# Optimization experiments

Hardware: AMD Instinct MI355X
Metric: run time of the kernel (lower is better)

## Reference

```python
import jax, jax.numpy as jnp
import numpy as np


def _up2(x):
    return jnp.repeat(jnp.repeat(x, 2, axis=2), 2, axis=3)


def setup_inputs() -> dict:
    key = jax.random.key(0)
    ks = jax.random.split(key, 6)
    Vps, C, H, W = 32, 128, 64, 64
    return {
        "x1": jax.random.normal(ks[0], (Vps, C, H, W), dtype=jnp.float32),
        "x2": jax.random.normal(ks[1], (Vps, C, H // 2, W // 2), dtype=jnp.float32),
        "x3": jax.random.normal(ks[2], (Vps, C, H // 4, W // 4), dtype=jnp.float32),
        "x4": jax.random.normal(ks[3], (Vps, C, H // 4, W // 4), dtype=jnp.float32),
        "conv_w": jax.random.normal(ks[4], (128, 512), dtype=jnp.float32) * 0.02,
        "conv_b": jnp.zeros((128,), dtype=jnp.float32),
        "gamma": jnp.zeros((1,), dtype=jnp.float32),
        "weight": jnp.ones((128,), dtype=jnp.float32),
        "lin_w": jax.random.normal(ks[5], (1, 128), dtype=jnp.float32) * 0.1,
    }


def reference(x1, x2, x3, x4, conv_w, conv_b, gamma, weight, lin_w):
    # upsample lower pyramid levels to x1 resolution and concat on channels
    x_sm = jnp.concatenate([x1, _up2(x2), _up2(_up2(x3)), _up2(_up2(x4))], axis=1)
    # 1x1 conv: [Vps,512,H,W] x [128,512] -> [Vps,128,H,W]
    x_sm = jnp.einsum('vchw,oc->vohw', x_sm, conv_w) + conv_b[None, :, None, None]
    Vps, C, H, W = x_sm.shape

    # --- batch (viewport) attention ---
    gap = jnp.mean(x_sm, axis=(2, 3))                     # [Vps, C]
    v_q = gap @ lin_w.T                                    # [Vps, 1]
    att = v_q @ v_q.T                                      # [Vps, Vps]
    att_new = jnp.broadcast_to(jnp.max(att, axis=-1, keepdims=True), att.shape)
    vps_mat = jax.nn.softmax(att_new, axis=-1)             # rows constant -> uniform
    v_v = x_sm.reshape(Vps, C * H * W)
    vps_att = (vps_mat @ v_v).reshape(Vps, C, H, W)
    x_sm = vps_att * gamma + x_sm

    # --- channel attention ---
    c_q = jnp.mean(x_sm, axis=(2, 3))                      # [Vps, C]
    att_C = c_q.T @ c_q                                    # [C, C]
    C_mat = jax.nn.softmax(att_C, axis=-1) * weight        # broadcast over last dim
    c_v = x_sm.reshape(C, Vps * H * W)                     # faithful raw reshape as in torch
    C_att = (C_mat @ c_v).reshape(Vps, C, H, W)
    out = C_att + x_sm
    return out.reshape(Vps, C, H * W)
```

## Files before the change

kernel.cpp:

```cpp
#include <hip/hip_runtime.h>

#define V 32
#define CH 128
#define SP 4096

typedef __attribute__((ext_vector_type(8))) short bf16x8;
typedef __attribute__((ext_vector_type(4))) float f32x4;

__device__ __forceinline__ unsigned short bf16rne(float x) {
    union { float f; unsigned u; } v; v.f = x;
    unsigned r = v.u + 0x7fff + ((v.u >> 16) & 1);
    return (unsigned short)(r >> 16);
}

__device__ __forceinline__ int xswz(int s) { return (s & 7) ^ ((s >> 2) & 7); }

__device__ __forceinline__ const float* xsm_row(const float* xsm, int j, int r) {
    return xsm + ((size_t)((j >> 2) * CH + (j & 3) * 32 + r)) * SP;
}

__global__ __launch_bounds__(256) void prep_w(const float* __restrict__ W,
                                              unsigned short* __restrict__ Wpad)
{
    int row = blockIdx.x;
    int j = threadIdx.x;
    if (j < 136) {
        int sigma = row >> 7, o = row & 127;
        float v = (j < 128) ? W[o * 512 + sigma * 128 + j] : 0.f;
        Wpad[row * 136 + j] = bf16rne(v);
    }
}

__global__ __launch_bounds__(256, 3) void conv_lo(
    const float* __restrict__ xa, const float* __restrict__ xb,
    const unsigned short* __restrict__ WA, const unsigned short* __restrict__ WB,
    int spatial, int nph, float* __restrict__ outbuf)
{
    __shared__ __align__(16) unsigned short Xl[64 * 128];
    const int v = blockIdx.y, sc = blockIdx.x, tid = threadIdx.x;
    const int lane = tid & 63, w = tid >> 6;
    const int l15 = lane & 15, quad = lane >> 4;
    const int o0 = (w >> 1) * 64, s0 = (w & 1) * 32;
    const int sq = tid & 15, cp0 = tid >> 4;

    f32x4 acc[4][2];
#pragma unroll
    for (int it = 0; it < 4; ++it)
#pragma unroll
        for (int st = 0; st < 2; ++st) acc[it][st] = (f32x4){0.f, 0.f, 0.f, 0.f};

#pragma unroll 1
    for (int ph = 0; ph < nph; ++ph) {
        if (ph) __syncthreads();
        const float* xp = ph ? xb : xa;
        const unsigned short* wp = ph ? WB : WA;
        bf16x8 af[4][4];
#pragma unroll
        for (int ks = 0; ks < 4; ++ks)
#pragma unroll
            for (int it = 0; it < 4; ++it)
                af[ks][it] = *(const bf16x8*)&wp[(o0 + it * 16 + l15) * 136 + ks * 32 + quad * 8];
        const float* xbase = xp + (size_t)v * CH * spatial + sc * 64;
#pragma unroll
        for (int rep = 0; rep < 4; ++rep) {
            int c = (cp0 + rep * 16) * 2;
            const float* r0 = xbase + (size_t)c * spatial + sq * 4;
            float4 va = *(const float4*)r0;
            float4 vb = *(const float4*)(r0 + spatial);
            float a4[4] = {va.x, va.y, va.z, va.w};
            float b4[4] = {vb.x, vb.y, vb.z, vb.w};
#pragma unroll
            for (int i = 0; i < 4; ++i) {
                int s = sq * 4 + i;
                ushort2 pk; pk.x = bf16rne(a4[i]); pk.y = bf16rne(b4[i]);
                *(ushort2*)&Xl[s * 128 + (((c >> 3) ^ xswz(s)) * 8) + (c & 7)] = pk;
            }
        }
        __syncthreads();
#pragma unroll
        for (int ks = 0; ks < 4; ++ks) {
            int kb = ks * 4 + quad;
            bf16x8 bfr[2];
#pragma unroll
            for (int st = 0; st < 2; ++st) {
                int s = s0 + st * 16 + l15;
                bfr[st] = *(const bf16x8*)&Xl[s * 128 + ((kb ^ xswz(s)) * 8)];
            }
#pragma unroll
            for (int it = 0; it < 4; ++it)
#pragma unroll
                for (int st = 0; st < 2; ++st)
                    acc[it][st] = __builtin_amdgcn_mfma_f32_16x16x32_bf16(
                        bfr[st], af[ks][it], acc[it][st], 0, 0, 0);
        }
    }
#pragma unroll
    for (int it = 0; it < 4; ++it) {
        int o = o0 + it * 16 + l15;
        float* orow = outbuf + ((size_t)(v * CH + o)) * spatial + sc * 64;
#pragma unroll
        for (int st = 0; st < 2; ++st) {
            int sb = s0 + st * 16 + quad * 4;
            *(f32x4*)(orow + sb) = acc[it][st];
        }
    }
}

__global__ __launch_bounds__(256, 2) void conv_full(
    const float* __restrict__ x1, const unsigned short* __restrict__ W0,
    const float* __restrict__ bias, const float* __restrict__ conv2,
    const float* __restrict__ conv34, float* __restrict__ xsm,
    float* __restrict__ gap)
{
    __shared__ __align__(16) unsigned short Xl[2][64 * 128];
    const int vg = blockIdx.y, sc = blockIdx.x, tid = threadIdx.x;
    const int lane = tid & 63, w = tid >> 6;
    const int l15 = lane & 15, quad = lane >> 4;
    const int o0 = (w >> 1) * 64, s0 = (w & 1) * 32;
    const int sq = tid & 15, cp0 = tid >> 4;

    bf16x8 af[4][4];
#pragma unroll
    for (int ks = 0; ks < 4; ++ks)
#pragma unroll
        for (int it = 0; it < 4; ++it)
            af[ks][it] = *(const bf16x8*)&W0[(o0 + it * 16 + l15) * 136 + ks * 32 + quad * 8];
    float bv[4];
#pragma unroll
    for (int it = 0; it < 4; ++it) bv[it] = bias[o0 + it * 16 + l15];

    float4 xva[4], xvb[4];
    {
        const float* xbase = x1 + (size_t)(vg * 4) * CH * SP + sc * 64;
#pragma unroll
        for (int rep = 0; rep < 4; ++rep) {
            int c = (cp0 + rep * 16) * 2;
            const float* r0 = xbase + (size_t)c * SP + sq * 4;
            xva[rep] = *(const float4*)r0;
            xvb[rep] = *(const float4*)(r0 + SP);
        }
    }
#pragma unroll
    for (int rep = 0; rep < 4; ++rep) {
        int c = (cp0 + rep * 16) * 2;
        float a4[4] = {xva[rep].x, xva[rep].y, xva[rep].z, xva[rep].w};
        float b4[4] = {xvb[rep].x, xvb[rep].y, xvb[rep].z, xvb[rep].w};
#pragma unroll
        for (int i = 0; i < 4; ++i) {
            int s = sq * 4 + i;
            ushort2 pk; pk.x = bf16rne(a4[i]); pk.y = bf16rne(b4[i]);
            *(ushort2*)&Xl[0][s * 128 + (((c >> 3) ^ xswz(s)) * 8) + (c & 7)] = pk;
        }
    }

#pragma unroll 1
    for (int t = 0; t < 4; ++t) {
        const int v = vg * 4 + t;
        __syncthreads();
        if (t < 3) {
            const float* xbase = x1 + (size_t)(v + 1) * CH * SP + sc * 64;
#pragma unroll
            for (int rep = 0; rep < 4; ++rep) {
                int c = (cp0 + rep * 16) * 2;
                const float* r0 = xbase + (size_t)c * SP + sq * 4;
                xva[rep] = *(const float4*)r0;
                xvb[rep] = *(const float4*)(r0 + SP);
            }
        }
        const float* c2row = conv2 + (size_t)v * CH * 1024 + (sc >> 1) * 32;
        const float* c34row = conv34 + (size_t)v * CH * 256 + (sc >> 2) * 16;
        float2 c2v[4][2]; float c34v[4][2];
#pragma unroll
        for (int it = 0; it < 4; ++it) {
            int o = o0 + it * 16 + l15;
#pragma unroll
            for (int st = 0; st < 2; ++st) {
                int sb = s0 + st * 16 + quad * 4;
                c2v[it][st] = *(const float2*)(c2row + (size_t)o * 1024 + (sb >> 1));
                c34v[it][st] = c34row[(size_t)o * 256 + (sb >> 2)];
            }
        }
        f32x4 acc[4][2];
#pragma unroll
        for (int it = 0; it < 4; ++it)
#pragma unroll
            for (int st = 0; st < 2; ++st) acc[it][st] = (f32x4){0.f, 0.f, 0.f, 0.f};
        const unsigned short* Xcur = &Xl[t & 1][0];
#pragma unroll
        for (int ks = 0; ks < 4; ++ks) {
            int kb = ks * 4 + quad;
            bf16x8 bfr[2];
#pragma unroll
            for (int st = 0; st < 2; ++st) {
                int s = s0 + st * 16 + l15;
                bfr[st] = *(const bf16x8*)&Xcur[s * 128 + ((kb ^ xswz(s)) * 8)];
            }
#pragma unroll
            for (int it = 0; it < 4; ++it)
#pragma unroll
                for (int st = 0; st < 2; ++st)
                    acc[it][st] = __builtin_amdgcn_mfma_f32_16x16x32_bf16(
                        bfr[st], af[ks][it], acc[it][st], 0, 0, 0);
        }
        float gs[4];
#pragma unroll
        for (int it = 0; it < 4; ++it) {
            int o = o0 + it * 16 + l15;
            float b = bv[it];
            float* orow = xsm + ((size_t)(v * CH + o)) * SP + sc * 64;
            float lsum = 0.f;
#pragma unroll
            for (int st = 0; st < 2; ++st) {
                int sb = s0 + st * 16 + quad * 4;
                f32x4 a = acc[it][st];
                f32x4 ov;
                ov[0] = a[0] + b + c2v[it][st].x + c34v[it][st];
                ov[1] = a[1] + b + c2v[it][st].x + c34v[it][st];
                ov[2] = a[2] + b + c2v[it][st].y + c34v[it][st];
                ov[3] = a[3] + b + c2v[it][st].y + c34v[it][st];
                *(f32x4*)(orow + sb) = ov;
                lsum += ov[0] + ov[1] + ov[2] + ov[3];
            }
            gs[it] = lsum;
        }
#pragma unroll
        for (int m = 16; m < 64; m <<= 1)
#pragma unroll
            for (int k = 0; k < 4; ++k) gs[k] += __shfl_xor(gs[k], m, 64);
        if (quad == 0) {
#pragma unroll
            for (int it = 0; it < 4; ++it)
                atomicAdd(&gap[v * CH + o0 + it * 16 + l15], gs[it]);
        }
        if (t < 3) {
#pragma unroll
            for (int rep = 0; rep < 4; ++rep) {
                int c = (cp0 + rep * 16) * 2;
                float a4[4] = {xva[rep].x, xva[rep].y, xva[rep].z, xva[rep].w};
                float b4[4] = {xvb[rep].x, xvb[rep].y, xvb[rep].z, xvb[rep].w};
#pragma unroll
                for (int i = 0; i < 4; ++i) {
                    int s = sq * 4 + i;
                    ushort2 pk; pk.x = bf16rne(a4[i]); pk.y = bf16rne(b4[i]);
                    *(ushort2*)&Xl[(t + 1) & 1][s * 128 + (((c >> 3) ^ xswz(s)) * 8) + (c & 7)] = pk;
                }
            }
        }
    }
}

__global__ __launch_bounds__(128) void build_G(
    const float* __restrict__ gap, const float* __restrict__ gammap,
    const float* __restrict__ weight, unsigned short* __restrict__ GsPad)
{
    __shared__ float cq[32][128];
    __shared__ float red[128];
    const int i = blockIdx.x, j = threadIdx.x;
    const float g = gammap[0];

    float gb = 0.f;
    for (int v = 0; v < 32; ++v) gb += gap[v * CH + j];
    gb = gb * (1.f / 32.f) * (1.f / 4096.f) * g;
    for (int v = 0; v < 32; ++v) cq[v][j] = gap[v * CH + j] * (1.f / 4096.f) + gb;
    __syncthreads();

    float a = 0.f;
    for (int v = 0; v < 32; ++v) a += cq[v][i] * cq[v][j];

    red[j] = a; __syncthreads();
    float m = -1e30f;
    for (int t = 0; t < 128; ++t) m = fmaxf(m, red[t]);
    __syncthreads();
    float e = __expf(a - m);
    red[j] = e; __syncthreads();
    float ssum = 0.f;
    for (int t = 0; t < 128; ++t) ssum += red[t];
    float cm = e / ssum * weight[j] + ((i == j) ? 1.f : 0.f);
    __syncthreads();
    red[j] = cm; __syncthreads();
    float rs = 0.f;
    for (int t = (j & 3); t < 128; t += 4) rs += red[t];
    float gfull = cm + g * (1.f / 32.f) * rs;
    GsPad[i * 136 + j] = bf16rne(gfull - ((i == j) ? 1.f : 0.f));
}

__global__ __launch_bounds__(256, 2) void apply_G(
    float* __restrict__ xsm, const unsigned short* __restrict__ GsPad)
{
    __shared__ __align__(16) unsigned short Xl[2][64 * 128];
    const int r = blockIdx.y, scg = blockIdx.x, tid = threadIdx.x;
    const int lane = tid & 63, w = tid >> 6;
    const int l15 = lane & 15, quad = lane >> 4;
    const int i0 = (w >> 1) * 64, s0 = (w & 1) * 32;
    const int sq = tid & 15, cp0 = tid >> 4;

    bf16x8 af[4][4];
#pragma unroll
    for (int ks = 0; ks < 4; ++ks)
#pragma unroll
        for (int it = 0; it < 4; ++it)
            af[ks][it] = *(const bf16x8*)&GsPad[(i0 + it * 16 + l15) * 136 + ks * 32 + quad * 8];

    float4 xva[4], xvb[4];
    {
        const int sc = scg * 4;
#pragma unroll
        for (int rep = 0; rep < 4; ++rep) {
            int c = (cp0 + rep * 16) * 2;
            xva[rep] = *(const float4*)(xsm_row(xsm, c, r) + sc * 64 + sq * 4);
            xvb[rep] = *(const float4*)(xsm_row(xsm, c + 1, r) + sc * 64 + sq * 4);
        }
    }
#pragma unroll
    for (int rep = 0; rep < 4; ++rep) {
        int c = (cp0 + rep * 16) * 2;
        float a4[4] = {xva[rep].x, xva[rep].y, xva[rep].z, xva[rep].w};
        float b4[4] = {xvb[rep].x, xvb[rep].y, xvb[rep].z, xvb[rep].w};
#pragma unroll
        for (int i = 0; i < 4; ++i) {
            int s = sq * 4 + i;
            ushort2 pk; pk.x = bf16rne(a4[i]); pk.y = bf16rne(b4[i]);
            *(ushort2*)&Xl[0][s * 128 + (((c >> 3) ^ xswz(s)) * 8) + (c & 7)] = pk;
        }
    }

#pragma unroll 1
    for (int t = 0; t < 4; ++t) {
        const int sc = scg * 4 + t;
        __syncthreads();
        if (t < 3) {
#pragma unroll
            for (int rep = 0; rep < 4; ++rep) {
                int c = (cp0 + rep * 16) * 2;
                xva[rep] = *(const float4*)(xsm_row(xsm, c, r) + (sc + 1) * 64 + sq * 4);
                xvb[rep] = *(const float4*)(xsm_row(xsm, c + 1, r) + (sc + 1) * 64 + sq * 4);
            }
        }
        f32x4 resv[4][2];
#pragma unroll
        for (int it = 0; it < 4; ++it) {
            int i = i0 + it * 16 + l15;
            const float* rowp = xsm_row(xsm, i, r) + sc * 64;
#pragma unroll
            for (int st = 0; st < 2; ++st) {
                int sb = s0 + st * 16 + quad * 4;
                resv[it][st] = *(const f32x4*)(rowp + sb);
            }
        }
        f32x4 acc[4][2];
#pragma unroll
        for (int it = 0; it < 4; ++it)
#pragma unroll
            for (int st = 0; st < 2; ++st) acc[it][st] = (f32x4){0.f, 0.f, 0.f, 0.f};
        const unsigned short* Xcur = &Xl[t & 1][0];
#pragma unroll
        for (int ks = 0; ks < 4; ++ks) {
            int kb = ks * 4 + quad;
            bf16x8 bfr[2];
#pragma unroll
            for (int st = 0; st < 2; ++st) {
                int s = s0 + st * 16 + l15;
                bfr[st] = *(const bf16x8*)&Xcur[s * 128 + ((kb ^ xswz(s)) * 8)];
            }
#pragma unroll
            for (int it = 0; it < 4; ++it)
#pragma unroll
                for (int st = 0; st < 2; ++st)
                    acc[it][st] = __builtin_amdgcn_mfma_f32_16x16x32_bf16(
                        bfr[st], af[ks][it], acc[it][st], 0, 0, 0);
        }
#pragma unroll
        for (int it = 0; it < 4; ++it) {
            int i = i0 + it * 16 + l15;
            float* rowp = (float*)xsm_row(xsm, i, r) + sc * 64;
#pragma unroll
            for (int st = 0; st < 2; ++st) {
                int sb = s0 + st * 16 + quad * 4;
                f32x4 res = resv[it][st] + acc[it][st];
                *(f32x4*)(rowp + sb) = res;
            }
        }
        if (t < 3) {
#pragma unroll
            for (int rep = 0; rep < 4; ++rep) {
                int c = (cp0 + rep * 16) * 2;
                float a4[4] = {xva[rep].x, xva[rep].y, xva[rep].z, xva[rep].w};
                float b4[4] = {xvb[rep].x, xvb[rep].y, xvb[rep].z, xvb[rep].w};
#pragma unroll
                for (int i = 0; i < 4; ++i) {
                    int s = sq * 4 + i;
                    ushort2 pk; pk.x = bf16rne(a4[i]); pk.y = bf16rne(b4[i]);
                    *(ushort2*)&Xl[(t + 1) & 1][s * 128 + (((c >> 3) ^ xswz(s)) * 8) + (c & 7)] = pk;
                }
            }
        }
    }
}

extern "C" void kernel_launch(void* const* d_in, const int* in_sizes, int n_in,
                              void* d_out, int out_size, void* d_ws, size_t ws_size,
                              hipStream_t stream)
{
    const float* x1     = (const float*)d_in[0];
    const float* x2     = (const float*)d_in[1];
    const float* x3     = (const float*)d_in[2];
    const float* x4     = (const float*)d_in[3];
    const float* conv_w = (const float*)d_in[4];
    const float* conv_b = (const float*)d_in[5];
    const float* gamma  = (const float*)d_in[6];
    const float* weight = (const float*)d_in[7];

    float* out = (float*)d_out;
    float* ws  = (float*)d_ws;

    float* conv2  = ws;
    float* conv34 = ws + (size_t)4194304;
    float* gap    = ws + (size_t)5242880;
    unsigned short* Wpad  = (unsigned short*)(ws + (size_t)5246976);
    unsigned short* GsPad = (unsigned short*)(ws + (size_t)5281792);

    hipMemsetAsync(gap, 0, 4096 * sizeof(float), stream);

    prep_w<<<512, 256, 0, stream>>>(conv_w, Wpad);
    conv_lo<<<dim3(16, 32), 256, 0, stream>>>(x2, x2, Wpad + 1 * 128 * 136,
                                              Wpad + 1 * 128 * 136, 1024, 1, conv2);
    conv_lo<<<dim3(4, 32), 256, 0, stream>>>(x3, x4, Wpad + 2 * 128 * 136,
                                             Wpad + 3 * 128 * 136, 256, 2, conv34);
    conv_full<<<dim3(64, 8), 256, 0, stream>>>(x1, Wpad, conv_b, conv2, conv34, out, gap);
    build_G<<<128, 128, 0, stream>>>(gap, gamma, weight, GsPad);
    apply_G<<<dim3(16, 32), 256, 0, stream>>>(out, GsPad);
}
```

Before: 238.3 us.

## Double block count in conv_full and apply_G, stage conv_lo weights in LDS

conv_full and apply_G now give each block two spatial tiles of one viewport instead of four tiles, doubling the grid to 1024 blocks with occupancy hint raised to 3. This should fill the GPU better and cut per-block register pressure. apply_G now reads the residual right before the store rather than prefetching it. conv_lo stages weights through shared memory instead of holding them in registers, swaps MFMA operand order, and writes output as scalar stores. The trade-off is less prefetch depth per block, and the scalar stores in conv_lo may coalesce poorly.

Result: slower. 346.9 us (+45.6%).

```diff
diff --git a/kernel.cpp b/kernel.cpp
--- a/kernel.cpp
+++ b/kernel.cpp
@@ -17,6 +17,23 @@
 
 __device__ __forceinline__ const float* xsm_row(const float* xsm, int j, int r) {
     return xsm + ((size_t)((j >> 2) * CH + (j & 3) * 32 + r)) * SP;
+}
+
+__device__ __forceinline__ void pack_tile(unsigned short* Xl, const float4* xva,
+                                          const float4* xvb, int sq, int cp0)
+{
+#pragma unroll
+    for (int rep = 0; rep < 4; ++rep) {
+        int c = (cp0 + rep * 16) * 2;
+        float a4[4] = {xva[rep].x, xva[rep].y, xva[rep].z, xva[rep].w};
+        float b4[4] = {xvb[rep].x, xvb[rep].y, xvb[rep].z, xvb[rep].w};
+#pragma unroll
+        for (int i = 0; i < 4; ++i) {
+            int s = sq * 4 + i;
+            ushort2 pk; pk.x = bf16rne(a4[i]); pk.y = bf16rne(b4[i]);
+            *(ushort2*)&Xl[s * 128 + (((c >> 3) ^ xswz(s)) * 8) + (c & 7)] = pk;
+        }
+    }
 }
 
 __global__ __launch_bounds__(256) void prep_w(const float* __restrict__ W,
@@ -31,11 +48,12 @@
     }
 }
 
-__global__ __launch_bounds__(256, 3) void conv_lo(
+__global__ __launch_bounds__(256) void conv_lo(
     const float* __restrict__ xa, const float* __restrict__ xb,
     const unsigned short* __restrict__ WA, const unsigned short* __restrict__ WB,
     int spatial, int nph, float* __restrict__ outbuf)
 {
+    __shared__ __align__(16) unsigned short Wl[128 * 136];
     __shared__ __align__(16) unsigned short Xl[64 * 128];
     const int v = blockIdx.y, sc = blockIdx.x, tid = threadIdx.x;
     const int lane = tid & 63, w = tid >> 6;
@@ -54,12 +72,11 @@
         if (ph) __syncthreads();
         const float* xp = ph ? xb : xa;
         const unsigned short* wp = ph ? WB : WA;
-        bf16x8 af[4][4];
-#pragma unroll
-        for (int ks = 0; ks < 4; ++ks)
-#pragma unroll
-            for (int it = 0; it < 4; ++it)
-                af[ks][it] = *(const bf16x8*)&wp[(o0 + it * 16 + l15) * 136 + ks * 32 + quad * 8];
+        {
+            const float4* wsrc = (const float4*)wp;
+            float4* wdst = (float4*)Wl;
+            for (int idx = tid; idx < 2176; idx += 256) wdst[idx] = wsrc[idx];
+        }
         const float* xbase = xp + (size_t)v * CH * spatial + sc * 64;
 #pragma unroll
         for (int rep = 0; rep < 4; ++rep) {
@@ -80,7 +97,10 @@
 #pragma unroll
         for (int ks = 0; ks < 4; ++ks) {
             int kb = ks * 4 + quad;
-            bf16x8 bfr[2];
+            bf16x8 af[4], bfr[2];
+#pragma unroll
+            for (int it = 0; it < 4; ++it)
+                af[it] = *(const bf16x8*)&Wl[(o0 + it * 16 + l15) * 136 + ks * 32 + quad * 8];
 #pragma unroll
             for (int st = 0; st < 2; ++st) {
                 int s = s0 + st * 16 + l15;
@@ -91,29 +111,31 @@
 #pragma unroll
                 for (int st = 0; st < 2; ++st)
                     acc[it][st] = __builtin_amdgcn_mfma_f32_16x16x32_bf16(
-                        bfr[st], af[ks][it], acc[it][st], 0, 0, 0);
-        }
-    }
-#pragma unroll
-    for (int it = 0; it < 4; ++it) {
-        int o = o0 + it * 16 + l15;
-        float* orow = outbuf + ((size_t)(v * CH + o)) * spatial + sc * 64;
-#pragma unroll
-        for (int st = 0; st < 2; ++st) {
-            int sb = s0 + st * 16 + quad * 4;
-            *(f32x4*)(orow + sb) = acc[it][st];
-        }
-    }
-}
-
-__global__ __launch_bounds__(256, 2) void conv_full(
+                        af[it], bfr[st], acc[it][st], 0, 0, 0);
+        }
+    }
+#pragma unroll
+    for (int it = 0; it < 4; ++it)
+#pragma unroll
+        for (int reg = 0; reg < 4; ++reg) {
+            int o = o0 + it * 16 + quad * 4 + reg;
+            float* orow = outbuf + ((size_t)(v * CH + o)) * spatial + sc * 64;
+#pragma unroll
+            for (int st = 0; st < 2; ++st) {
+                int s_l = s0 + st * 16 + l15;
+                orow[s_l] = acc[it][st][reg];
+            }
+        }
+}
+
+__global__ __launch_bounds__(256, 3) void conv_full(
     const float* __restrict__ x1, const unsigned short* __restrict__ W0,
     const float* __restrict__ bias, const float* __restrict__ conv2,
     const float* __restrict__ conv34, float* __restrict__ xsm,
     float* __restrict__ gap)
 {
     __shared__ __align__(16) unsigned short Xl[2][64 * 128];
-    const int vg = blockIdx.y, sc = blockIdx.x, tid = threadIdx.x;
+    const int v = blockIdx.y, scp = blockIdx.x, tid = threadIdx.x;
     const int lane = tid & 63, w = tid >> 6;
     const int l15 = lane & 15, quad = lane >> 4;
     const int o0 = (w >> 1) * 64, s0 = (w & 1) * 32;
@@ -129,43 +151,30 @@
 #pragma unroll
     for (int it = 0; it < 4; ++it) bv[it] = bias[o0 + it * 16 + l15];
 
+    const float* xbase0 = x1 + (size_t)v * CH * SP + (scp * 2) * 64;
     float4 xva[4], xvb[4];
-    {
-        const float* xbase = x1 + (size_t)(vg * 4) * CH * SP + sc * 64;
-#pragma unroll
-        for (int rep = 0; rep < 4; ++rep) {
-            int c = (cp0 + rep * 16) * 2;
-            const float* r0 = xbase + (size_t)c * SP + sq * 4;
-            xva[rep] = *(const float4*)r0;
-            xvb[rep] = *(const float4*)(r0 + SP);
-        }
-    }
 #pragma unroll
     for (int rep = 0; rep < 4; ++rep) {
         int c = (cp0 + rep * 16) * 2;
-        float a4[4] = {xva[rep].x, xva[rep].y, xva[rep].z, xva[rep].w};
-        float b4[4] = {xvb[rep].x, xvb[rep].y, xvb[rep].z, xvb[rep].w};
-#pragma unroll
-        for (int i = 0; i < 4; ++i) {
-            int s = sq * 4 + i;
-            ushort2 pk; pk.x = bf16rne(a4[i]); pk.y = bf16rne(b4[i]);
-            *(ushort2*)&Xl[0][s * 128 + (((c >> 3) ^ xswz(s)) * 8) + (c & 7)] = pk;
-        }
-    }
+        const float* r0 = xbase0 + (size_t)c * SP + sq * 4;
+        xva[rep] = *(const float4*)r0;
+        xvb[rep] = *(const float4*)(r0 + SP);
+    }
+    pack_tile(&Xl[0][0], xva, xvb, sq, cp0);
+    __syncthreads();
 
 #pragma unroll 1
-    for (int t = 0; t < 4; ++t) {
-        const int v = vg * 4 + t;
-        __syncthreads();
-        if (t < 3) {
-            const float* xbase = x1 + (size_t)(v + 1) * CH * SP + sc * 64;
+    for (int t = 0; t < 2; ++t) {
+        const int sc = scp * 2 + t;
+        if (t == 0) {
 #pragma unroll
             for (int rep = 0; rep < 4; ++rep) {
                 int c = (cp0 + rep * 16) * 2;
-                const float* r0 = xbase + (size_t)c * SP + sq * 4;
+                const float* r0 = xbase0 + 64 + (size_t)c * SP + sq * 4;
                 xva[rep] = *(const float4*)r0;
                 xvb[rep] = *(const float4*)(r0 + SP);
             }
+            __builtin_amdgcn_sched_barrier(0);
         }
         const float* c2row = conv2 + (size_t)v * CH * 1024 + (sc >> 1) * 32;
         const float* c34row = conv34 + (size_t)v * CH * 256 + (sc >> 2) * 16;
@@ -185,7 +194,7 @@
         for (int it = 0; it < 4; ++it)
 #pragma unroll
             for (int st = 0; st < 2; ++st) acc[it][st] = (f32x4){0.f, 0.f, 0.f, 0.f};
-        const unsigned short* Xcur = &Xl[t & 1][0];
+        const unsigned short* Xcur = &Xl[t][0];
 #pragma unroll
         for (int ks = 0; ks < 4; ++ks) {
             int kb = ks * 4 + quad;
@@ -232,19 +241,9 @@
             for (int it = 0; it < 4; ++it)
                 atomicAdd(&gap[v * CH + o0 + it * 16 + l15], gs[it]);
         }
-        if (t < 3) {
-#pragma unroll
-            for (int rep = 0; rep < 4; ++rep) {
-                int c = (cp0 + rep * 16) * 2;
-                float a4[4] = {xva[rep].x, xva[rep].y, xva[rep].z, xva[rep].w};
-                float b4[4] = {xvb[rep].x, xvb[rep].y, xvb[rep].z, xvb[rep].w};
-#pragma unroll
-                for (int i = 0; i < 4; ++i) {
-                    int s = sq * 4 + i;
-                    ushort2 pk; pk.x = bf16rne(a4[i]); pk.y = bf16rne(b4[i]);
-                    *(ushort2*)&Xl[(t + 1) & 1][s * 128 + (((c >> 3) ^ xswz(s)) * 8) + (c & 7)] = pk;
-                }
-            }
+        if (t == 0) {
+            pack_tile(&Xl[1][0], xva, xvb, sq, cp0);
+            __syncthreads();
         }
     }
 }
@@ -284,11 +283,11 @@
     GsPad[i * 136 + j] = bf16rne(gfull - ((i == j) ? 1.f : 0.f));
 }
 
-__global__ __launch_bounds__(256, 2) void apply_G(
+__global__ __launch_bounds__(256, 3) void apply_G(
     float* __restrict__ xsm, const unsigned short* __restrict__ GsPad)
 {
     __shared__ __align__(16) unsigned short Xl[2][64 * 128];
-    const int r = blockIdx.y, scg = blockIdx.x, tid = threadIdx.x;
+    const int r = blockIdx.y, scp = blockIdx.x, tid = threadIdx.x;
     const int lane = tid & 63, w = tid >> 6;
     const int l15 = lane & 15, quad = lane >> 4;
     const int i0 = (w >> 1) * 64, s0 = (w & 1) * 32;
@@ -302,57 +301,33 @@
             af[ks][it] = *(const bf16x8*)&GsPad[(i0 + it * 16 + l15) * 136 + ks * 32 + quad * 8];
 
     float4 xva[4], xvb[4];
-    {
-        const int sc = scg * 4;
-#pragma unroll
-        for (int rep = 0; rep < 4; ++rep) {
-            int c = (cp0 + rep * 16) * 2;
-            xva[rep] = *(const float4*)(xsm_row(xsm, c, r) + sc * 64 + sq * 4);
-            xvb[rep] = *(const float4*)(xsm_row(xsm, c + 1, r) + sc * 64 + sq * 4);
-        }
-    }
 #pragma unroll
     for (int rep = 0; rep < 4; ++rep) {
         int c = (cp0 + rep * 16) * 2;
-        float a4[4] = {xva[rep].x, xva[rep].y, xva[rep].z, xva[rep].w};
-        float b4[4] = {xvb[rep].x, xvb[rep].y, xvb[rep].z, xvb[rep].w};
-#pragma unroll
-        for (int i = 0; i < 4; ++i) {
-            int s = sq * 4 + i;
-            ushort2 pk; pk.x = bf16rne(a4[i]); pk.y = bf16rne(b4[i]);
-            *(ushort2*)&Xl[0][s * 128 + (((c >> 3) ^ xswz(s)) * 8) + (c & 7)] = pk;
-        }
-    }
+        xva[rep] = *(const float4*)(xsm_row(xsm, c, r) + (scp * 2) * 64 + sq * 4);
+        xvb[rep] = *(const float4*)(xsm_row(xsm, c + 1, r) + (scp * 2) * 64 + sq * 4);
+    }
+    pack_tile(&Xl[0][0], xva, xvb, sq, cp0);
+    __syncthreads();
 
 #pragma unroll 1
-    for (int t = 0; t < 4; ++t) {
-        const int sc = scg * 4 + t;
-        __syncthreads();
-        if (t < 3) {
+    for (int t = 0; t < 2; ++t) {
+        const int sc = scp * 2 + t;
+        if (t == 0) {
 #pragma unroll
             for (int rep = 0; rep < 4; ++rep) {
                 int c = (cp0 + rep * 16) * 2;
                 xva[rep] = *(const float4*)(xsm_row(xsm, c, r) + (sc + 1) * 64 + sq * 4);
                 xvb[rep] = *(const float4*)(xsm_row(xsm, c + 1, r) + (sc + 1) * 64 + sq * 4);
             }
-        }
-        f32x4 resv[4][2];
-#pragma unroll
-        for (int it = 0; it < 4; ++it) {
-            int i = i0 + it * 16 + l15;
-            const float* rowp = xsm_row(xsm, i, r) + sc * 64;
-#pragma unroll
-            for (int st = 0; st < 2; ++st) {
-                int sb = s0 + st * 16 + quad * 4;
-                resv[it][st] = *(const f32x4*)(rowp + sb);
-            }
+            __builtin_amdgcn_sched_barrier(0);
         }
         f32x4 acc[4][2];
 #pragma unroll
         for (int it = 0; it < 4; ++it)
 #pragma unroll
             for (int st = 0; st < 2; ++st) acc[it][st] = (f32x4){0.f, 0.f, 0.f, 0.f};
-        const unsigned short* Xcur = &Xl[t & 1][0];
+        const unsigned short* Xcur = &Xl[t][0];
 #pragma unroll
         for (int ks = 0; ks < 4; ++ks) {
             int kb = ks * 4 + quad;
@@ -376,23 +351,14 @@
 #pragma unroll
             for (int st = 0; st < 2; ++st) {
                 int sb = s0 + st * 16 + quad * 4;
-                f32x4 res = resv[it][st] + acc[it][st];
+                f32x4 res = *(const f32x4*)(rowp + sb);
+                res += acc[it][st];
                 *(f32x4*)(rowp + sb) = res;
             }
         }
-        if (t < 3) {
-#pragma unroll
-            for (int rep = 0; rep < 4; ++rep) {
-                int c = (cp0 + rep * 16) * 2;
-                float a4[4] = {xva[rep].x, xva[rep].y, xva[rep].z, xva[rep].w};
-                float b4[4] = {xvb[rep].x, xvb[rep].y, xvb[rep].z, xvb[rep].w};
-#pragma unroll
-                for (int i = 0; i < 4; ++i) {
-                    int s = sq * 4 + i;
-                    ushort2 pk; pk.x = bf16rne(a4[i]); pk.y = bf16rne(b4[i]);
-                    *(ushort2*)&Xl[(t + 1) & 1][s * 128 + (((c >> 3) ^ xswz(s)) * 8) + (c & 7)] = pk;
-                }
-            }
+        if (t == 0) {
+            pack_tile(&Xl[1][0], xva, xvb, sq, cp0);
+            __syncthreads();
         }
     }
 }
@@ -426,7 +392,7 @@
                                               Wpad + 1 * 128 * 136, 1024, 1, conv2);
     conv_lo<<<dim3(4, 32), 256, 0, stream>>>(x3, x4, Wpad + 2 * 128 * 136,
                                              Wpad + 3 * 128 * 136, 256, 2, conv34);
-    conv_full<<<dim3(64, 8), 256, 0, stream>>>(x1, Wpad, conv_b, conv2, conv34, out, gap);
+    conv_full<<<dim3(32, 32), 256, 0, stream>>>(x1, Wpad, conv_b, conv2, conv34, out, gap);
     build_G<<<128, 128, 0, stream>>>(gap, gamma, weight, GsPad);
-    apply_G<<<dim3(16, 32), 256, 0, stream>>>(out, GsPad);
-}
+    apply_G<<<dim3(32, 32), 256, 0, stream>>>(out, GsPad);
+}
```
